# Performance work log

Measured on AMD Instinct MI355X. Metric: run time of the kernel, lower is better.

Reference implementation:

```python
import jax, jax.numpy as jnp
import numpy as np

S, T, H, D = 4096, 4096, 16, 64
N_EMBD = H * D

def setup_inputs() -> dict:
    key = jax.random.key(0)
    kq, kk, kv, kw = jax.random.split(key, 4)
    q = jax.random.normal(kq, (S, H, D), dtype=jnp.float32)
    k = jax.random.normal(kk, (T, H, D), dtype=jnp.float32)
    v = jax.random.normal(kv, (T, H, D), dtype=jnp.float32)
    # GPT-2 style init: std = 0.02 / sqrt(2 * n_layer), n_layer = 24
    W_proj = jax.random.normal(kw, (N_EMBD, N_EMBD), dtype=jnp.float32) * (0.02 / np.sqrt(2 * 24))
    return {"q": q, "k": k, "v": v, "W_proj": W_proj}

def reference(q, k, v, W_proj):
    s, h, d = q.shape
    t = k.shape[0]
    # causal bias: mask positions where query index < key index (future keys)
    causal_bias = (jnp.arange(s)[:, None] < jnp.arange(t)[None, :]).astype(jnp.float32) * -10000.0
    scale = 1.0 / jnp.sqrt(jnp.float32(d))
    # [h, s, t] scores in fp32 (matches original .astype(jnp.float32))
    scores = jnp.einsum('shd,thd->hst', q, k).astype(jnp.float32) * scale + causal_bias
    attn = jax.nn.softmax(scores, axis=-1).astype(q.dtype)
    # dropout p=0 / inference -> identity
    out = jnp.einsum('hst,thd->shd', attn, v).reshape(s, h * d)
    # nn.Linear (no bias) vmapped over tokens: y = x @ W.T
    return out @ W_proj.T
```

## Files before the change

kernel.cpp:

```cpp
#include <hip/hip_runtime.h>

#define S_LEN 4096
#define NH 16
#define DH 64
#define NE 1024

typedef __bf16 bf16_t;
typedef __bf16 bf16x8 __attribute__((ext_vector_type(8)));
typedef __bf16 bf16x4 __attribute__((ext_vector_type(4)));
typedef float  f32x4  __attribute__((ext_vector_type(4)));

#define QSCALE 0.180336879f

__global__ __launch_bounds__(256) void pack_qkw(const float* __restrict__ q,
                                                const float* __restrict__ k,
                                                const float* __restrict__ w,
                                                bf16_t* __restrict__ qb,
                                                bf16_t* __restrict__ kb,
                                                bf16_t* __restrict__ wb) {
    const int tid = blockIdx.x * 256 + threadIdx.x;
    const int e = tid * 4;
    const int s = e >> 10;
    const int c = e & (NE - 1);
    const int h = c >> 6;
    const int d = c & (DH - 1);
    const int o = (h * S_LEN + s) * DH + d;
    float4 qv = *(const float4*)(q + e);
    float4 kv = *(const float4*)(k + e);
    bf16x4 qo, ko;
    qo[0] = (bf16_t)(qv.x * QSCALE); qo[1] = (bf16_t)(qv.y * QSCALE);
    qo[2] = (bf16_t)(qv.z * QSCALE); qo[3] = (bf16_t)(qv.w * QSCALE);
    ko[0] = (bf16_t)kv.x; ko[1] = (bf16_t)kv.y; ko[2] = (bf16_t)kv.z; ko[3] = (bf16_t)kv.w;
    *(bf16x4*)(qb + o) = qo;
    *(bf16x4*)(kb + o) = ko;
    if (tid < (NE * NE / 4)) {
        float4 wv = *(const float4*)(w + tid * 4);
        bf16x4 wo;
        wo[0] = (bf16_t)wv.x; wo[1] = (bf16_t)wv.y; wo[2] = (bf16_t)wv.z; wo[3] = (bf16_t)wv.w;
        *(bf16x4*)(wb + tid * 4) = wo;
    }
}

__global__ __launch_bounds__(256) void pack_vt(const float* __restrict__ v,
                                               bf16_t* __restrict__ vt) {
    __shared__ bf16_t tile[64][65];
    const int h  = blockIdx.y;
    const int t0 = blockIdx.x * 64;
    const int r  = threadIdx.x >> 6;
    const int cl = threadIdx.x & 63;
#pragma unroll
    for (int rep = 0; rep < 16; ++rep) {
        int i = rep * 4 + r;
        tile[cl][i] = (bf16_t)v[(t0 + i) * NE + h * DH + cl];
    }
    __syncthreads();
#pragma unroll
    for (int rep = 0; rep < 16; ++rep) {
        int d = rep * 4 + r;
        vt[(h * DH + d) * S_LEN + t0 + cl] = tile[d][cl];
    }
}

__global__ __launch_bounds__(512, 4) void attn(const bf16_t* __restrict__ qb,
                                               const bf16_t* __restrict__ kb,
                                               const bf16_t* __restrict__ vt,
                                               float* __restrict__ po,
                                               float* __restrict__ ls) {
    __shared__ __align__(16) bf16_t kbuf[2][64 * 72];
    __shared__ __align__(16) bf16_t vbuf[2][64 * 72];
    __shared__ __align__(16) bf16_t pbuf[8][16 * 72];

    const int tid  = threadIdx.x;
    const int wave = tid >> 6;
    const int lane = tid & 63;
    const int l15  = lane & 15;
    const int quad = lane >> 4;
    const int h = blockIdx.x;
    const int x = blockIdx.y;

    const int sA = x;
    const int sB = 31 - x;
    const int n0 = x + 1;
    const int b1 = sB + 1;
    const int N  = 33;

    const bf16_t* __restrict__ qh = qb + h * (S_LEN * DH);
    const bf16_t* __restrict__ kh = kb + h * (S_LEN * DH);
    const bf16_t* __restrict__ vh = vt + h * (DH * S_LEN);

    const int row0 = tid >> 3;
    const int tc8  = (tid & 7) * 8;

    f32x4 o_acc[4];
    float lsum[4];
    bf16x8 qA[2];
    int s0 = sA * 128 + wave * 16;

    auto load_q = [&](int s0_) {
#pragma unroll
        for (int dc = 0; dc < 2; ++dc)
            qA[dc] = *(const bf16x8*)(qh + (s0_ + l15) * DH + dc * 32 + quad * 8);
    };
    auto reset_acc = [&]() {
#pragma unroll
        for (int db = 0; db < 4; ++db) o_acc[db] = (f32x4){0.f, 0.f, 0.f, 0.f};
#pragma unroll
        for (int r = 0; r < 4; ++r) lsum[r] = 0.0f;
    };
    auto epilogue = [&](int s0_, int slot) {
        float l2[4];
#pragma unroll
        for (int r = 0; r < 4; ++r) l2[r] = lsum[r];
#pragma unroll
        for (int off = 8; off >= 1; off >>= 1)
#pragma unroll
            for (int r = 0; r < 4; ++r) l2[r] += __shfl_xor(l2[r], off, 64);
        float* poz = po + (size_t)(slot * NH + h) * S_LEN * DH;
#pragma unroll
        for (int db = 0; db < 4; ++db)
#pragma unroll
            for (int r = 0; r < 4; ++r)
                poz[(s0_ + quad * 4 + r) * DH + db * 16 + l15] = o_acc[db][r];
        if (l15 == 0) {
            float* lsz = ls + (size_t)(slot * NH + h) * S_LEN;
#pragma unroll
            for (int r = 0; r < 4; ++r) lsz[s0_ + quad * 4 + r] = l2[r];
        }
    };

    load_q(s0);
    reset_acc();

    {
        bf16x8 kr = *(const bf16x8*)(kh + row0 * DH + tc8);
        bf16x8 vr = *(const bf16x8*)(vh + row0 * S_LEN + tc8);
        *(bf16x8*)(kbuf[0] + row0 * 72 + tc8) = kr;
        *(bf16x8*)(vbuf[0] + row0 * 72 + tc8) = vr;
    }
    __syncthreads();

    for (int j = 0; j < N; ++j) {
        if (j == n0) {
            epilogue(s0, 0);
            s0 = sB * 128 + wave * 16;
            load_q(s0);
            reset_acc();
        }
        const int t0 = (j < n0 ? j : b1 + (j - n0)) * 64;
        const bf16_t* kb_ = kbuf[j & 1];
        const bf16_t* vb_ = vbuf[j & 1];

        bf16x8 krn, vrn;
        const bool pf = (j + 1 < N);
        if (pf) {
            const int jn = j + 1;
            const int tn = (jn < n0 ? jn : b1 + (jn - n0)) * 64;
            krn = *(const bf16x8*)(kh + (tn + row0) * DH + tc8);
            vrn = *(const bf16x8*)(vh + row0 * S_LEN + tn + tc8);
        }

        f32x4 c_[4];
#pragma unroll
        for (int ch = 0; ch < 4; ++ch) {
            bf16x8 kB0 = *(const bf16x8*)(kb_ + (ch * 16 + l15) * 72 + quad * 8);
            bf16x8 kB1 = *(const bf16x8*)(kb_ + (ch * 16 + l15) * 72 + 32 + quad * 8);
            f32x4 zr = (f32x4){0.f, 0.f, 0.f, 0.f};
            zr = __builtin_amdgcn_mfma_f32_16x16x32_bf16(qA[0], kB0, zr, 0, 0, 0);
            zr = __builtin_amdgcn_mfma_f32_16x16x32_bf16(qA[1], kB1, zr, 0, 0, 0);
            c_[ch] = zr;
        }

        if (t0 + 63 > s0) {
#pragma unroll
            for (int ch = 0; ch < 4; ++ch) {
                int col = t0 + ch * 16 + l15;
#pragma unroll
                for (int r = 0; r < 4; ++r) {
                    int row = s0 + quad * 4 + r;
                    if (col > row) c_[ch][r] = -INFINITY;
                }
            }
        }

        bf16_t* pl = pbuf[wave];
#pragma unroll
        for (int ch = 0; ch < 4; ++ch)
#pragma unroll
            for (int r = 0; r < 4; ++r) {
                float p = exp2f(c_[ch][r] - 17.0f);
                lsum[r] += p;
                pl[(quad * 4 + r) * 72 + ch * 16 + l15] = (bf16_t)p;
            }

        __builtin_amdgcn_wave_barrier();

        bf16x8 pA[2];
#pragma unroll
        for (int kc = 0; kc < 2; ++kc)
            pA[kc] = *(const bf16x8*)(pbuf[wave] + l15 * 72 + kc * 32 + quad * 8);

        bf16x8 vB[4][2];
#pragma unroll
        for (int db = 0; db < 4; ++db)
#pragma unroll
            for (int kc = 0; kc < 2; ++kc)
                vB[db][kc] = *(const bf16x8*)(vb_ + (db * 16 + l15) * 72 + kc * 32 + quad * 8);

#pragma unroll
        for (int db = 0; db < 4; ++db) {
            o_acc[db] = __builtin_amdgcn_mfma_f32_16x16x32_bf16(pA[0], vB[db][0], o_acc[db], 0, 0, 0);
            o_acc[db] = __builtin_amdgcn_mfma_f32_16x16x32_bf16(pA[1], vB[db][1], o_acc[db], 0, 0, 0);
        }

        if (pf) {
            *(bf16x8*)(kbuf[(j + 1) & 1] + row0 * 72 + tc8) = krn;
            *(bf16x8*)(vbuf[(j + 1) & 1] + row0 * 72 + tc8) = vrn;
        }
        __syncthreads();
    }

    epilogue(s0, 1);
}

__global__ __launch_bounds__(256) void combine(const float* __restrict__ po,
                                               const float* __restrict__ ls,
                                               bf16_t* __restrict__ xb) {
    const int idx = blockIdx.x * 256 + threadIdx.x;
    const int row = idx >> 8;
    const int c   = (idx & 255) * 4;
    const int h   = c >> 6;
    const int d   = c & 63;
    const size_t base0 = (size_t)(h) * S_LEN * DH + row * DH + d;
    const size_t base1 = (size_t)(NH + h) * S_LEN * DH + row * DH + d;
    float4 o0 = *(const float4*)(po + base0);
    float4 o1 = *(const float4*)(po + base1);
    float l = ls[(size_t)h * S_LEN + row] + ls[(size_t)(NH + h) * S_LEN + row];
    float inv = 1.0f / l;
    bf16x4 out;
    out[0] = (bf16_t)((o0.x + o1.x) * inv);
    out[1] = (bf16_t)((o0.y + o1.y) * inv);
    out[2] = (bf16_t)((o0.z + o1.z) * inv);
    out[3] = (bf16_t)((o0.w + o1.w) * inv);
    *(bf16x4*)(xb + (size_t)row * NE + c) = out;
}

__global__ __launch_bounds__(256, 4) void proj(const bf16_t* __restrict__ xb,
                                               const bf16_t* __restrict__ wb,
                                               float* __restrict__ y) {
    __shared__ __align__(16) bf16_t wbuf[2][64 * 72];
    const int tid  = threadIdx.x;
    const int wave = tid >> 6;
    const int lane = tid & 63;
    const int l15  = lane & 15;
    const int quad = lane >> 4;
    const int m0 = blockIdx.x * 128 + wave * 32;
    const int n0 = blockIdx.y * 64;

    const int row0 = tid >> 3;
    const int tc8  = (tid & 7) * 8;

    f32x4 acc[2][4];
#pragma unroll
    for (int rf = 0; rf < 2; ++rf)
#pragma unroll
        for (int nb = 0; nb < 4; ++nb) acc[rf][nb] = (f32x4){0.f, 0.f, 0.f, 0.f};

    {
        bf16x8 wr0 = *(const bf16x8*)(wb + (n0 + row0) * NE + tc8);
        bf16x8 wr1 = *(const bf16x8*)(wb + (n0 + row0 + 32) * NE + tc8);
        *(bf16x8*)(wbuf[0] + row0 * 72 + tc8) = wr0;
        *(bf16x8*)(wbuf[0] + (row0 + 32) * 72 + tc8) = wr1;
    }
    bf16x8 a[2][2];
#pragma unroll
    for (int rf = 0; rf < 2; ++rf)
#pragma unroll
        for (int kc = 0; kc < 2; ++kc)
            a[rf][kc] = *(const bf16x8*)(xb + (m0 + rf * 16 + l15) * NE + kc * 32 + quad * 8);
    __syncthreads();

    for (int kt = 0; kt < 16; ++kt) {
        const bf16_t* wb_ = wbuf[kt & 1];
        const bool pf = (kt + 1 < 16);
        bf16x8 wr0, wr1, an[2][2];
        if (pf) {
            const int kn = (kt + 1) * 64;
            wr0 = *(const bf16x8*)(wb + (n0 + row0) * NE + kn + tc8);
            wr1 = *(const bf16x8*)(wb + (n0 + row0 + 32) * NE + kn + tc8);
#pragma unroll
            for (int rf = 0; rf < 2; ++rf)
#pragma unroll
                for (int kc = 0; kc < 2; ++kc)
                    an[rf][kc] = *(const bf16x8*)(xb + (m0 + rf * 16 + l15) * NE + kn + kc * 32 + quad * 8);
        }

#pragma unroll
        for (int nb = 0; nb < 4; ++nb)
#pragma unroll
            for (int kc = 0; kc < 2; ++kc) {
                bf16x8 b = *(const bf16x8*)(wb_ + (nb * 16 + l15) * 72 + kc * 32 + quad * 8);
                acc[0][nb] = __builtin_amdgcn_mfma_f32_16x16x32_bf16(a[0][kc], b, acc[0][nb], 0, 0, 0);
                acc[1][nb] = __builtin_amdgcn_mfma_f32_16x16x32_bf16(a[1][kc], b, acc[1][nb], 0, 0, 0);
            }

        if (pf) {
            *(bf16x8*)(wbuf[(kt + 1) & 1] + row0 * 72 + tc8) = wr0;
            *(bf16x8*)(wbuf[(kt + 1) & 1] + (row0 + 32) * 72 + tc8) = wr1;
#pragma unroll
            for (int rf = 0; rf < 2; ++rf)
#pragma unroll
                for (int kc = 0; kc < 2; ++kc) a[rf][kc] = an[rf][kc];
        }
        __syncthreads();
    }

#pragma unroll
    for (int rf = 0; rf < 2; ++rf)
#pragma unroll
        for (int nb = 0; nb < 4; ++nb)
#pragma unroll
            for (int r = 0; r < 4; ++r)
                y[(m0 + rf * 16 + quad * 4 + r) * NE + n0 + nb * 16 + l15] = acc[rf][nb][r];
}

extern "C" void kernel_launch(void* const* d_in, const int* in_sizes, int n_in,
                              void* d_out, int out_size, void* d_ws, size_t ws_size,
                              hipStream_t stream) {
    const float* q = (const float*)d_in[0];
    const float* k = (const float*)d_in[1];
    const float* v = (const float*)d_in[2];
    const float* w = (const float*)d_in[3];
    float* y = (float*)d_out;

    bf16_t* ws = (bf16_t*)d_ws;
    bf16_t* qb = ws;
    bf16_t* kb = qb + 4 * 1024 * 1024;
    bf16_t* vt = kb + 4 * 1024 * 1024;
    bf16_t* wb = vt + 4 * 1024 * 1024;
    bf16_t* xb = wb + 1024 * 1024;
    float*  po = (float*)(xb + 4 * 1024 * 1024);
    float*  ls = po + (size_t)2 * NH * S_LEN * DH;

    pack_qkw<<<dim3(4096), dim3(256), 0, stream>>>(q, k, w, qb, kb, wb);
    pack_vt<<<dim3(S_LEN / 64, NH), dim3(256), 0, stream>>>(v, vt);
    attn<<<dim3(NH, 32), dim3(512), 0, stream>>>(qb, kb, vt, po, ls);
    combine<<<dim3(4096), dim3(256), 0, stream>>>(po, ls, xb);
    proj<<<dim3(S_LEN / 128, NE / 64), dim3(256), 0, stream>>>(xb, wb, y);
}
```

Measured before the change: 198.7 us.

## Merge pack kernels into one launch and halve proj M-tile

New measurement: 198.5 us. No clear change (-0.1%).

```diff
diff --git a/kernel.cpp b/kernel.cpp
--- a/kernel.cpp
+++ b/kernel.cpp
@@ -8,56 +8,65 @@
 typedef __bf16 bf16_t;
 typedef __bf16 bf16x8 __attribute__((ext_vector_type(8)));
 typedef __bf16 bf16x4 __attribute__((ext_vector_type(4)));
+typedef __bf16 bf16x2 __attribute__((ext_vector_type(2)));
 typedef float  f32x4  __attribute__((ext_vector_type(4)));
 
 #define QSCALE 0.180336879f
 
-__global__ __launch_bounds__(256) void pack_qkw(const float* __restrict__ q,
+__global__ __launch_bounds__(256) void pack_all(const float* __restrict__ q,
                                                 const float* __restrict__ k,
                                                 const float* __restrict__ w,
+                                                const float* __restrict__ v,
                                                 bf16_t* __restrict__ qb,
                                                 bf16_t* __restrict__ kb,
-                                                bf16_t* __restrict__ wb) {
-    const int tid = blockIdx.x * 256 + threadIdx.x;
-    const int e = tid * 4;
-    const int s = e >> 10;
-    const int c = e & (NE - 1);
-    const int h = c >> 6;
-    const int d = c & (DH - 1);
-    const int o = (h * S_LEN + s) * DH + d;
-    float4 qv = *(const float4*)(q + e);
-    float4 kv = *(const float4*)(k + e);
-    bf16x4 qo, ko;
-    qo[0] = (bf16_t)(qv.x * QSCALE); qo[1] = (bf16_t)(qv.y * QSCALE);
-    qo[2] = (bf16_t)(qv.z * QSCALE); qo[3] = (bf16_t)(qv.w * QSCALE);
-    ko[0] = (bf16_t)kv.x; ko[1] = (bf16_t)kv.y; ko[2] = (bf16_t)kv.z; ko[3] = (bf16_t)kv.w;
-    *(bf16x4*)(qb + o) = qo;
-    *(bf16x4*)(kb + o) = ko;
-    if (tid < (NE * NE / 4)) {
-        float4 wv = *(const float4*)(w + tid * 4);
-        bf16x4 wo;
-        wo[0] = (bf16_t)wv.x; wo[1] = (bf16_t)wv.y; wo[2] = (bf16_t)wv.z; wo[3] = (bf16_t)wv.w;
-        *(bf16x4*)(wb + tid * 4) = wo;
-    }
-}
-
-__global__ __launch_bounds__(256) void pack_vt(const float* __restrict__ v,
-                                               bf16_t* __restrict__ vt) {
+                                                bf16_t* __restrict__ wb,
+                                                bf16_t* __restrict__ vt) {
     __shared__ bf16_t tile[64][65];
-    const int h  = blockIdx.y;
-    const int t0 = blockIdx.x * 64;
-    const int r  = threadIdx.x >> 6;
-    const int cl = threadIdx.x & 63;
-#pragma unroll
-    for (int rep = 0; rep < 16; ++rep) {
-        int i = rep * 4 + r;
-        tile[cl][i] = (bf16_t)v[(t0 + i) * NE + h * DH + cl];
-    }
-    __syncthreads();
-#pragma unroll
-    for (int rep = 0; rep < 16; ++rep) {
-        int d = rep * 4 + r;
-        vt[(h * DH + d) * S_LEN + t0 + cl] = tile[d][cl];
+    const int bid = blockIdx.x;
+    if (bid < 4096) {
+        const int tid = bid * 256 + threadIdx.x;
+        const int e = tid * 4;
+        const int s = e >> 10;
+        const int c = e & (NE - 1);
+        const int h = c >> 6;
+        const int d = c & (DH - 1);
+        const int o = (h * S_LEN + s) * DH + d;
+        float4 qv = *(const float4*)(q + e);
+        float4 kv = *(const float4*)(k + e);
+        bf16x4 qo, ko;
+        qo[0] = (bf16_t)(qv.x * QSCALE); qo[1] = (bf16_t)(qv.y * QSCALE);
+        qo[2] = (bf16_t)(qv.z * QSCALE); qo[3] = (bf16_t)(qv.w * QSCALE);
+        ko[0] = (bf16_t)kv.x; ko[1] = (bf16_t)kv.y; ko[2] = (bf16_t)kv.z; ko[3] = (bf16_t)kv.w;
+        *(bf16x4*)(qb + o) = qo;
+        *(bf16x4*)(kb + o) = ko;
+        if (tid < (NE * NE / 4)) {
+            float4 wv = *(const float4*)(w + tid * 4);
+            bf16x4 wo;
+            wo[0] = (bf16_t)wv.x; wo[1] = (bf16_t)wv.y; wo[2] = (bf16_t)wv.z; wo[3] = (bf16_t)wv.w;
+            *(bf16x4*)(wb + tid * 4) = wo;
+        }
+    } else {
+        const int vb = bid - 4096;
+        const int h  = vb >> 6;
+        const int t0 = (vb & 63) * 64;
+        const int r  = threadIdx.x >> 6;
+        const int cl = threadIdx.x & 63;
+#pragma unroll
+        for (int rep = 0; rep < 16; ++rep) {
+            int i = rep * 4 + r;
+            tile[cl][i] = (bf16_t)v[(t0 + i) * NE + h * DH + cl];
+        }
+        __syncthreads();
+        const int r2  = threadIdx.x >> 5;
+        const int cl2 = (threadIdx.x & 31) * 2;
+#pragma unroll
+        for (int rep = 0; rep < 8; ++rep) {
+            int d = rep * 8 + r2;
+            bf16x2 out;
+            out[0] = tile[d][cl2];
+            out[1] = tile[d][cl2 + 1];
+            *(bf16x2*)(vt + (h * DH + d) * S_LEN + t0 + cl2) = out;
+        }
     }
 }
 
@@ -253,17 +262,15 @@
     const int lane = tid & 63;
     const int l15  = lane & 15;
     const int quad = lane >> 4;
-    const int m0 = blockIdx.x * 128 + wave * 32;
+    const int m0 = blockIdx.x * 64 + wave * 16;
     const int n0 = blockIdx.y * 64;
 
     const int row0 = tid >> 3;
     const int tc8  = (tid & 7) * 8;
 
-    f32x4 acc[2][4];
-#pragma unroll
-    for (int rf = 0; rf < 2; ++rf)
-#pragma unroll
-        for (int nb = 0; nb < 4; ++nb) acc[rf][nb] = (f32x4){0.f, 0.f, 0.f, 0.f};
+    f32x4 acc[4];
+#pragma unroll
+    for (int nb = 0; nb < 4; ++nb) acc[nb] = (f32x4){0.f, 0.f, 0.f, 0.f};
 
     {
         bf16x8 wr0 = *(const bf16x8*)(wb + (n0 + row0) * NE + tc8);
@@ -271,27 +278,23 @@
         *(bf16x8*)(wbuf[0] + row0 * 72 + tc8) = wr0;
         *(bf16x8*)(wbuf[0] + (row0 + 32) * 72 + tc8) = wr1;
     }
-    bf16x8 a[2][2];
-#pragma unroll
-    for (int rf = 0; rf < 2; ++rf)
-#pragma unroll
-        for (int kc = 0; kc < 2; ++kc)
-            a[rf][kc] = *(const bf16x8*)(xb + (m0 + rf * 16 + l15) * NE + kc * 32 + quad * 8);
+    bf16x8 a[2];
+#pragma unroll
+    for (int kc = 0; kc < 2; ++kc)
+        a[kc] = *(const bf16x8*)(xb + (m0 + l15) * NE + kc * 32 + quad * 8);
     __syncthreads();
 
     for (int kt = 0; kt < 16; ++kt) {
         const bf16_t* wb_ = wbuf[kt & 1];
         const bool pf = (kt + 1 < 16);
-        bf16x8 wr0, wr1, an[2][2];
+        bf16x8 wr0, wr1, an[2];
         if (pf) {
             const int kn = (kt + 1) * 64;
             wr0 = *(const bf16x8*)(wb + (n0 + row0) * NE + kn + tc8);
             wr1 = *(const bf16x8*)(wb + (n0 + row0 + 32) * NE + kn + tc8);
 #pragma unroll
-            for (int rf = 0; rf < 2; ++rf)
-#pragma unroll
-                for (int kc = 0; kc < 2; ++kc)
-                    an[rf][kc] = *(const bf16x8*)(xb + (m0 + rf * 16 + l15) * NE + kn + kc * 32 + quad * 8);
+            for (int kc = 0; kc < 2; ++kc)
+                an[kc] = *(const bf16x8*)(xb + (m0 + l15) * NE + kn + kc * 32 + quad * 8);
         }
 
 #pragma unroll
@@ -299,28 +302,23 @@
 #pragma unroll
             for (int kc = 0; kc < 2; ++kc) {
                 bf16x8 b = *(const bf16x8*)(wb_ + (nb * 16 + l15) * 72 + kc * 32 + quad * 8);
-                acc[0][nb] = __builtin_amdgcn_mfma_f32_16x16x32_bf16(a[0][kc], b, acc[0][nb], 0, 0, 0);
-                acc[1][nb] = __builtin_amdgcn_mfma_f32_16x16x32_bf16(a[1][kc], b, acc[1][nb], 0, 0, 0);
+                acc[nb] = __builtin_amdgcn_mfma_f32_16x16x32_bf16(a[kc], b, acc[nb], 0, 0, 0);
             }
 
         if (pf) {
             *(bf16x8*)(wbuf[(kt + 1) & 1] + row0 * 72 + tc8) = wr0;
             *(bf16x8*)(wbuf[(kt + 1) & 1] + (row0 + 32) * 72 + tc8) = wr1;
 #pragma unroll
-            for (int rf = 0; rf < 2; ++rf)
-#pragma unroll
-                for (int kc = 0; kc < 2; ++kc) a[rf][kc] = an[rf][kc];
+            for (int kc = 0; kc < 2; ++kc) a[kc] = an[kc];
         }
         __syncthreads();
     }
 
 #pragma unroll
-    for (int rf = 0; rf < 2; ++rf)
-#pragma unroll
-        for (int nb = 0; nb < 4; ++nb)
-#pragma unroll
-            for (int r = 0; r < 4; ++r)
-                y[(m0 + rf * 16 + quad * 4 + r) * NE + n0 + nb * 16 + l15] = acc[rf][nb][r];
+    for (int nb = 0; nb < 4; ++nb)
+#pragma unroll
+        for (int r = 0; r < 4; ++r)
+            y[(m0 + quad * 4 + r) * NE + n0 + nb * 16 + l15] = acc[nb][r];
 }
 
 extern "C" void kernel_launch(void* const* d_in, const int* in_sizes, int n_in,
@@ -341,9 +339,8 @@
     float*  po = (float*)(xb + 4 * 1024 * 1024);
     float*  ls = po + (size_t)2 * NH * S_LEN * DH;
 
-    pack_qkw<<<dim3(4096), dim3(256), 0, stream>>>(q, k, w, qb, kb, wb);
-    pack_vt<<<dim3(S_LEN / 64, NH), dim3(256), 0, stream>>>(v, vt);
+    pack_all<<<dim3(4096 + 1024), dim3(256), 0, stream>>>(q, k, w, v, qb, kb, wb, vt);
     attn<<<dim3(NH, 32), dim3(512), 0, stream>>>(qb, kb, vt, po, ls);
     combine<<<dim3(4096), dim3(256), 0, stream>>>(po, ls, xb);
-    proj<<<dim3(S_LEN / 128, NE / 64), dim3(256), 0, stream>>>(xb, wb, y);
-}
+    proj<<<dim3(S_LEN / 64, NE / 64), dim3(256), 0, stream>>>(xb, wb, y);
+}
```
